# Performance work log

Hardware: AMD Instinct MI355X
Metric: run time of the kernel (lower is better)

The kernel has to match this reference:

```python
import jax, jax.numpy as jnp
import numpy as np

R = 4  # box-filter radius (init kwarg 'radious')


def _diff(c, r, axis):
    # c: cumulative sum along `axis`; returns box-sum along that axis.
    n = c.shape[axis]
    sl = lambda a, b: jax.lax.slice_in_dim(c, a, b, axis=axis)
    left = sl(r, 2 * r + 1)
    middle = sl(2 * r + 1, n) - sl(0, n - 2 * r - 1)
    right = sl(n - 1, n) - sl(n - 2 * r - 1, n - r - 1)
    return jnp.concatenate([left, middle, right], axis=axis)


def _box_filter(x, r):
    # cumsum along H (axis 2) -> windowed diff along H,
    # then cumsum along W (axis 3) -> windowed diff along W.
    return _diff(jnp.cumsum(_diff(jnp.cumsum(x, axis=2), r, axis=2), axis=3), r, axis=3)


def setup_inputs() -> dict:
    key = jax.random.key(0)
    x = jax.random.uniform(key, (8, 3, 1024, 1024), dtype=jnp.float32)
    return {"x": x}


def reference(x) -> jnp.ndarray:
    return _box_filter(x, R)
```

## Files before the change

kernel.cpp:

```cpp
#include <hip/hip_runtime.h>


constexpr int H = 1024, W = 1024;
constexpr int RAD = 4;
constexpr int OUTW = 248;
constexpr int NSTRIP = 5;
constexpr int CHUNK = 16;
constexpr int NCHUNK = H / CHUNK;
constexpr int NIMG = 24;
constexpr int NROWS = CHUNK + 2 * RAD + 1;

__global__ __launch_bounds__(256) void box9_kernel(const float* __restrict__ x,
                                                   float* __restrict__ out) {
    const int lane = threadIdx.x & 63;
    const int wid  = blockIdx.x * 4 + (threadIdx.x >> 6);

    const int chunk = wid & (NCHUNK - 1);
    const int t     = wid >> 6;
    const int strip = t % NSTRIP;
    const int img   = t / NSTRIP;

    const int  cs  = strip * OUTW - RAD + lane * 4;
    const bool cok = (cs >= 0) && (cs + 3 < W);
    const float* xp = x   + (size_t)img * (H * W) + (cok ? cs : 0);
    float*       op = out + (size_t)img * (H * W) + (cok ? cs : 0);

    const int h0 = chunk * CHUNK;

    float4 r[NROWS];
#pragma unroll
    for (int j = 0; j < NROWS; ++j) {
        const int row = h0 - RAD + j;
        r[j] = (cok && (unsigned)row < (unsigned)H)
             ? *reinterpret_cast<const float4*>(xp + (size_t)row * W)
             : make_float4(0.f, 0.f, 0.f, 0.f);
    }

    float4 V = make_float4(0.f, 0.f, 0.f, 0.f);
#pragma unroll
    for (int j = 0; j < 9; ++j) {
        V.x += r[j].x; V.y += r[j].y; V.z += r[j].z; V.w += r[j].w;
    }

    const bool sok = cok && (lane >= 1) && (lane <= 62);

#pragma unroll
    for (int j = 0; j < CHUNK; ++j) {
        const float p0 = V.x, p1 = p0 + V.y, p2 = p1 + V.z, T = p2 + V.w;
        const float s3 = V.w, s2 = s3 + V.z, s1 = s2 + V.y;
        const float L0 = __shfl(T,  lane - 1);
        const float L1 = __shfl(s1, lane - 1);
        const float L2 = __shfl(s2, lane - 1);
        const float L3 = __shfl(s3, lane - 1);
        const float R0 = __shfl(p0, lane + 1);
        const float R1 = __shfl(p1, lane + 1);
        const float R2 = __shfl(p2, lane + 1);
        const float R3 = __shfl(T,  lane + 1);
        float4 o;
        o.x = L0 + T + R0;
        o.y = L1 + T + R1;
        o.z = L2 + T + R2;
        o.w = L3 + T + R3;
        if (sok) *reinterpret_cast<float4*>(op + (size_t)(h0 + j) * W) = o;

        V.x += r[j + 9].x - r[j].x;
        V.y += r[j + 9].y - r[j].y;
        V.z += r[j + 9].z - r[j].z;
        V.w += r[j + 9].w - r[j].w;
    }
}

extern "C" void kernel_launch(void* const* d_in, const int* in_sizes, int n_in,
                              void* d_out, int out_size, void* d_ws, size_t ws_size,
                              hipStream_t stream) {
    const float* x   = (const float*)d_in[0];
    float*       out = (float*)d_out;
    const int n_waves  = NIMG * NSTRIP * NCHUNK;
    const int n_blocks = n_waves / 4;
    box9_kernel<<<dim3(n_blocks), dim3(256), 0, stream>>>(x, out);
}
```

Before: 39.27 us.

## Cover full row width per block using LDS halo exchange instead of overlapping wave strips

Each 256-thread block now covers an entire 1024-wide row band (four floats per thread), replacing five overlapping 248-wide strips handled per wave. The horizontal neighbour exchange moves from wave shuffles to a double-buffered shared-memory array with a block barrier per output row. This removes the redundant halo loads and the idle edge lanes of the strip layout. In exchange it adds a __syncthreads and LDS traffic on every one of the 16 rows.

```diff
diff --git a/kernel.cpp b/kernel.cpp
--- a/kernel.cpp
+++ b/kernel.cpp
@@ -3,35 +3,39 @@
 
 constexpr int H = 1024, W = 1024;
 constexpr int RAD = 4;
-constexpr int OUTW = 248;
-constexpr int NSTRIP = 5;
 constexpr int CHUNK = 16;
 constexpr int NCHUNK = H / CHUNK;
 constexpr int NIMG = 24;
 constexpr int NROWS = CHUNK + 2 * RAD + 1;
+constexpr int TPB = 256;
 
-__global__ __launch_bounds__(256) void box9_kernel(const float* __restrict__ x,
+__global__ __launch_bounds__(TPB) void box9_kernel(const float* __restrict__ x,
                                                    float* __restrict__ out) {
-    const int lane = threadIdx.x & 63;
-    const int wid  = blockIdx.x * 4 + (threadIdx.x >> 6);
+    __shared__ float4 Vs[2][TPB + 2];
 
-    const int chunk = wid & (NCHUNK - 1);
-    const int t     = wid >> 6;
-    const int strip = t % NSTRIP;
-    const int img   = t / NSTRIP;
+    const int t     = threadIdx.x;
+    const int bid   = blockIdx.x;
+    const int chunk = bid & (NCHUNK - 1);
+    const int img   = bid >> 6;
 
-    const int  cs  = strip * OUTW - RAD + lane * 4;
-    const bool cok = (cs >= 0) && (cs + 3 < W);
-    const float* xp = x   + (size_t)img * (H * W) + (cok ? cs : 0);
-    float*       op = out + (size_t)img * (H * W) + (cok ? cs : 0);
+    const float* xp = x   + (size_t)img * (H * W) + 4 * t;
+    float*       op = out + (size_t)img * (H * W) + 4 * t;
+    const int h0 = chunk * CHUNK;
 
-    const int h0 = chunk * CHUNK;
+    if (t == 0) {
+        Vs[0][0] = make_float4(0.f, 0.f, 0.f, 0.f);
+        Vs[1][0] = make_float4(0.f, 0.f, 0.f, 0.f);
+    }
+    if (t == TPB - 1) {
+        Vs[0][TPB + 1] = make_float4(0.f, 0.f, 0.f, 0.f);
+        Vs[1][TPB + 1] = make_float4(0.f, 0.f, 0.f, 0.f);
+    }
 
     float4 r[NROWS];
 #pragma unroll
     for (int j = 0; j < NROWS; ++j) {
         const int row = h0 - RAD + j;
-        r[j] = (cok && (unsigned)row < (unsigned)H)
+        r[j] = ((unsigned)row < (unsigned)H)
              ? *reinterpret_cast<const float4*>(xp + (size_t)row * W)
              : make_float4(0.f, 0.f, 0.f, 0.f);
     }
@@ -42,26 +46,30 @@
         V.x += r[j].x; V.y += r[j].y; V.z += r[j].z; V.w += r[j].w;
     }
 
-    const bool sok = cok && (lane >= 1) && (lane <= 62);
-
 #pragma unroll
     for (int j = 0; j < CHUNK; ++j) {
-        const float p0 = V.x, p1 = p0 + V.y, p2 = p1 + V.z, T = p2 + V.w;
-        const float s3 = V.w, s2 = s3 + V.z, s1 = s2 + V.y;
-        const float L0 = __shfl(T,  lane - 1);
-        const float L1 = __shfl(s1, lane - 1);
-        const float L2 = __shfl(s2, lane - 1);
-        const float L3 = __shfl(s3, lane - 1);
-        const float R0 = __shfl(p0, lane + 1);
-        const float R1 = __shfl(p1, lane + 1);
-        const float R2 = __shfl(p2, lane + 1);
-        const float R3 = __shfl(T,  lane + 1);
+        const int buf = j & 1;
+        Vs[buf][t + 1] = V;
+        __syncthreads();
+        const float4 VL = Vs[buf][t];
+        const float4 VR = Vs[buf][t + 2];
+
+        const float T   = V.x + V.y + V.z + V.w;
+        const float ls3 = VL.w;
+        const float ls2 = ls3 + VL.z;
+        const float ls1 = ls2 + VL.y;
+        const float lT  = ls1 + VL.x;
+        const float rp0 = VR.x;
+        const float rp1 = rp0 + VR.y;
+        const float rp2 = rp1 + VR.z;
+        const float rT  = rp2 + VR.w;
+
         float4 o;
-        o.x = L0 + T + R0;
-        o.y = L1 + T + R1;
-        o.z = L2 + T + R2;
-        o.w = L3 + T + R3;
-        if (sok) *reinterpret_cast<float4*>(op + (size_t)(h0 + j) * W) = o;
+        o.x = lT  + T + rp0;
+        o.y = ls1 + T + rp1;
+        o.z = ls2 + T + rp2;
+        o.w = ls3 + T + rT;
+        *reinterpret_cast<float4*>(op + (size_t)(h0 + j) * W) = o;
 
         V.x += r[j + 9].x - r[j].x;
         V.y += r[j + 9].y - r[j].y;
@@ -75,7 +83,6 @@
                               hipStream_t stream) {
     const float* x   = (const float*)d_in[0];
     float*       out = (float*)d_out;
-    const int n_waves  = NIMG * NSTRIP * NCHUNK;
-    const int n_blocks = n_waves / 4;
-    box9_kernel<<<dim3(n_blocks), dim3(256), 0, stream>>>(x, out);
+    const int n_blocks = NIMG * NCHUNK;
+    box9_kernel<<<dim3(n_blocks), dim3(TPB), 0, stream>>>(x, out);
 }
```

Result: slower. 42.37 us (+7.9%).
